# Optimization experiments

Hardware: AMD Instinct MI355X
Metric: run time of the kernel (lower is better)

## Reference

```python
import jax, jax.numpy as jnp
import numpy as np

B, H, W = 64, 512, 512
CD = 400                      # center_dims
MS_H = MS_W = 10              # max shifts
EPS = 1e-8
C_X = (H - CD) // 2           # 56
C_Y = (W - CD) // 2           # 56


def _conv_valid(x, k):
    # x: [B,h,w,1], k: [kh,kw,1,1] -> VALID conv, stride 1
    return jax.lax.conv_general_dilated(
        x, k, window_strides=(1, 1), padding='VALID',
        dimension_numbers=('NHWC', 'HWIO', 'NHWC'))


def setup_inputs() -> dict:
    key = jax.random.key(0)
    k1, k2 = jax.random.split(key)
    # smooth low-frequency template (so NCC peak neighborhood is positive -> log() finite)
    coarse = jax.random.normal(k1, (32, 32), dtype=jnp.float32)
    template = jax.image.resize(coarse, (H, W), method='bilinear')
    template = template - template.min() + 1.0  # keep positive-ish intensities
    noise = 0.05 * jax.random.normal(k2, (B, H, W, 1), dtype=jnp.float32)
    x = template[None, :, :, None] + noise
    return {'x': x, 'template': template}


def reference(x, template):
    # --- template normalization (init-time in the TF layer) ---
    tmpl = template[MS_W + C_X: H - (MS_W + C_X), MS_H + C_Y: W - (MS_H + C_Y)]  # [380,380]
    tmpl = tmpl[:, :, None, None].astype(jnp.float32)                            # HWIO
    t_zm = tmpl - jnp.mean(tmpl, axis=(0, 1), keepdims=True)
    t_var = jnp.sum(jnp.square(t_zm), axis=(0, 1), keepdims=True) + EPS          # [1,1,1,1]

    # --- image normalization ---
    Xc = x[:, C_X:H - C_X, C_Y:W - C_Y, :]                                       # [B,400,400,1]
    imgs_zm = Xc - jnp.mean(Xc, axis=(1, 2), keepdims=True)
    ones_k = jnp.ones_like(tmpl)
    localsum_sq = _conv_valid(jnp.square(Xc), ones_k)                            # [B,21,21,1]
    localsum = _conv_valid(Xc, ones_k)
    n_t = float(np.prod(tmpl.shape))
    imgs_var = localsum_sq - jnp.square(localsum) / n_t + EPS
    imgs_var = jnp.where(imgs_var < 0, jnp.zeros_like(imgs_var), imgs_var)

    # --- NCC ---
    denominator = jnp.sqrt(t_var * imgs_var)
    numerator = _conv_valid(imgs_zm, t_zm)
    ncc = numerator / denominator
    ncc = jnp.where(jnp.isnan(ncc), jnp.zeros_like(ncc), ncc)                    # [B,21,21,1]

    # --- integer argmax + gaussian (log-parabola) subpixel interpolation ---
    ncc2 = ncc[..., 0]                                                           # [B,21,21]
    ww = ncc2.shape[2]
    am = jnp.argmax(ncc2.reshape(B, -1), axis=1)
    sh_x = (am // ww).astype(jnp.int32)
    sh_y = (am % ww).astype(jnp.int32)
    log_ncc = jnp.log(ncc2)
    bidx = jnp.arange(B)

    def g(dx, dy):
        return log_ncc[bidx, sh_x + dx, sh_y + dy]

    log_xm1_y = g(-1, 0); log_xp1_y = g(1, 0)
    log_x_ym1 = g(0, -1); log_x_yp1 = g(0, 1)
    four_log_xy = 4.0 * g(0, 0)
    sh_x_n = (-(sh_x - MS_H)).astype(jnp.float32) - (log_xm1_y - log_xp1_y) / (
        2.0 * log_xm1_y - four_log_xy + 2.0 * log_xp1_y)
    sh_y_n = (-(sh_y - MS_W)).astype(jnp.float32) - (log_x_ym1 - log_x_yp1) / (
        2.0 * log_x_ym1 - four_log_xy + 2.0 * log_x_yp1)

    # --- bilinear translate: translations=[dx,dy]=[sh_y_n, sh_x_n]; out(r,c)=in(r-dy, c-dx), fill 0 ---
    def warp_one(img, dy, dx):
        rr = jnp.arange(H, dtype=jnp.float32)[:, None] - dy    # [H,1]
        cc = jnp.arange(W, dtype=jnp.float32)[None, :] - dx    # [1,W]
        r0 = jnp.floor(rr); c0 = jnp.floor(cc)
        wr = rr - r0; wc = cc - c0
        r0i = jnp.broadcast_to(r0.astype(jnp.int32), (H, W))
        c0i = jnp.broadcast_to(c0.astype(jnp.int32), (H, W))

        def samp(ri, ci):
            valid = (ri >= 0) & (ri < H) & (ci >= 0) & (ci < W)
            v = img[jnp.clip(ri, 0, H - 1), jnp.clip(ci, 0, W - 1)]
            return jnp.where(valid, v, 0.0)

        v00 = samp(r0i, c0i); v01 = samp(r0i, c0i + 1)
        v10 = samp(r0i + 1, c0i); v11 = samp(r0i + 1, c0i + 1)
        return (v00 * (1 - wr) * (1 - wc) + v01 * (1 - wr) * wc
                + v10 * wr * (1 - wc) + v11 * wr * wc)

    warped = jax.vmap(warp_one)(x[..., 0], sh_x_n, sh_y_n)     # [B,H,W]
    # transpose [0,2,1] then flatten, matching the TF layer's output layout
    return jnp.transpose(warped, (0, 2, 1)).reshape(B, H * W)
```

## Files before the change

### kernel.cpp

```cpp
#include <hip/hip_runtime.h>
#include <math.h>

#define HH 512
#define WW 512
#define NB 64
#define CXY 56
#define TOFF 66
#define TN 380
#define XN 400
#define NL 21
#define N_T 144400.0f
#define EPSF 1e-8f
#define NUT 32
#define SXS 424

#define TPART_S   0
#define TPART_S2  384
#define TSTATS    768
#define ROWSUM    1024
#define ROWSUMSQ  (ROWSUM + 537600)
#define LOCALSUM  1076224
#define LOCALSQ   (LOCALSUM + 28224)
#define SHIFTS    1132672
#define SHIFTSI   (SHIFTS + 128)
#define EXACTN    (SHIFTSI + 128)
#define TSHIFT_F  (EXACTN + 384)
#define XF16      (TSHIFT_F + 1677312)
#define CCPART2   8348416

typedef _Float16 half2_t __attribute__((ext_vector_type(2)));
typedef _Float16 f16x8 __attribute__((ext_vector_type(8)));
typedef float f32x4 __attribute__((ext_vector_type(4)));

__global__ __launch_bounds__(128) void k_tstats1(const float* __restrict__ tpl,
                                                 float* __restrict__ ws) {
    int u = blockIdx.x;
    int l = threadIdx.x;
    const float* row = tpl + (TOFF + u) * WW + TOFF;
    float s = 0.f, s2 = 0.f;
    for (int v = l; v < TN; v += 128) { float t = row[v]; s += t; s2 += t * t; }
    for (int off = 32; off; off >>= 1) { s += __shfl_down(s, off); s2 += __shfl_down(s2, off); }
    __shared__ float rs[2], rs2[2];
    int wid = l >> 6;
    if ((l & 63) == 0) { rs[wid] = s; rs2[wid] = s2; }
    __syncthreads();
    if (l == 0) { ws[TPART_S + u] = rs[0] + rs[1]; ws[TPART_S2 + u] = rs2[0] + rs2[1]; }
}

__global__ __launch_bounds__(512) void k_tstats2(float* __restrict__ ws) {
    int l = threadIdx.x;
    float s  = (l < TN) ? ws[TPART_S + l]  : 0.f;
    float s2 = (l < TN) ? ws[TPART_S2 + l] : 0.f;
    for (int off = 32; off; off >>= 1) { s += __shfl_down(s, off); s2 += __shfl_down(s2, off); }
    __shared__ float rs[8], rs2[8];
    int wid = l >> 6;
    if ((l & 63) == 0) { rs[wid] = s; rs2[wid] = s2; }
    __syncthreads();
    if (l == 0) {
        float S = 0.f, S2 = 0.f;
        for (int k = 0; k < 8; ++k) { S += rs[k]; S2 += rs2[k]; }
        float mu = S / N_T;
        ws[TSTATS] = mu;
        ws[TSTATS + 1] = S2 - S * mu + EPSF;
    }
}

__global__ __launch_bounds__(256) void k_tshift(const float* __restrict__ tpl,
                                                float* __restrict__ ws) {
    int u = blockIdx.x;
    int j = blockIdx.y;
    float mu = ws[TSTATS];
    _Float16* dst = (_Float16*)(ws + TSHIFT_F) + ((size_t)j * 384 + u) * 416;
    for (int c = threadIdx.x; c < 416; c += 256) {
        float v = 0.f;
        int vs = c - j;
        if (u < TN && vs >= 0 && vs < TN) v = tpl[(TOFF + u) * WW + TOFF + vs] - mu;
        dst[c] = (_Float16)v;
    }
}

__global__ __launch_bounds__(256) void k_rowsum(const float* __restrict__ x,
                                                float* __restrict__ ws) {
    __shared__ float sm[4][416];
    int wid = threadIdx.x >> 6, lane = threadIdx.x & 63;
    int row = blockIdx.x * 4 + wid;
    int b = row / 416, p = row - b * 416;
    const float* xr = x + ((size_t)b * HH + (CXY + p)) * WW + CXY;
    _Float16* xh = (_Float16*)(ws + XF16) + ((size_t)b * 416 + p) * 416;
    float s = 0.f, s2 = 0.f;
    for (int v = lane; v < 416; v += 64) {
        float t = xr[v];
        sm[wid][v] = t;
        xh[v] = (_Float16)t;
        if (v < TN) { s += t; s2 += t * t; }
    }
    for (int off = 32; off; off >>= 1) { s += __shfl_down(s, off); s2 += __shfl_down(s2, off); }
    __syncthreads();
    if (lane == 0 && p < XN) {
        float* rs  = ws + ROWSUM   + (size_t)(b * XN + p) * NL;
        float* rq  = ws + ROWSUMSQ + (size_t)(b * XN + p) * NL;
        float w = s, w2 = s2;
        rs[0] = w; rq[0] = w2;
        for (int j = 1; j < NL; ++j) {
            float a = sm[wid][j - 1], bv = sm[wid][j + TN - 1];
            w  += bv - a;
            w2 += bv * bv - a * a;
            rs[j] = w; rq[j] = w2;
        }
    }
}

__global__ __launch_bounds__(512) void k_ccm(float* __restrict__ ws) {
    const int bp = blockIdx.x, ut = blockIdx.y;
    const int U = 12 * ut;
    const int tid = threadIdx.x;
    const int lane = tid & 63, wv = tid >> 6;
    __shared__ __align__(16) _Float16 sX[2][32 * SXS];
    __shared__ float sD[7][16][34];

    {
        const _Float16* xh = (const _Float16*)(ws + XF16);
#pragma unroll
        for (int bb = 0; bb < 2; ++bb) {
            const _Float16* src0 = xh + ((size_t)(2 * bp + bb) * 416 + U) * 416;
            for (int c = tid; c < 32 * 52; c += 512) {
                int r = c / 52, c8 = c - r * 52;
                *reinterpret_cast<f16x8*>(&sX[bb][r * SXS + c8 * 8]) =
                    *reinterpret_cast<const f16x8*>(src0 + (size_t)r * 416 + c8 * 8);
            }
        }
    }
    __syncthreads();

    if (wv < 7) {
        const _Float16* tsh = (const _Float16*)(ws + TSHIFT_F);
        const int r16 = lane & 15, h8 = (lane >> 4) * 8;
        const int rbase = (lane >> 4) * 4, cbase = lane & 15;
        const _Float16* bbA = &sX[0][r16 * SXS + h8];
        const _Float16* bbB = &sX[1][r16 * SXS + h8];

        const int j0 = 3 * wv;
        const _Float16* a0 = tsh + ((size_t)(j0    ) * 384 + U + r16) * 416 + h8;
        const _Float16* a1 = tsh + ((size_t)(j0 + 1) * 384 + U + r16) * 416 + h8;
        const _Float16* a2 = tsh + ((size_t)(j0 + 2) * 384 + U + r16) * 416 + h8;

        f32x4 z = {0.f, 0.f, 0.f, 0.f};
        f32x4 c000 = z, c001 = z, c010 = z, c011 = z, c020 = z, c021 = z;
        f32x4 c100 = z, c101 = z, c110 = z, c111 = z, c120 = z, c121 = z;
        f16x8 A0 = *reinterpret_cast<const f16x8*>(a0);
        f16x8 A1 = *reinterpret_cast<const f16x8*>(a1);
        f16x8 A2 = *reinterpret_cast<const f16x8*>(a2);
#pragma unroll
        for (int kc = 0; kc < 13; ++kc) {
            f16x8 N0 = A0, N1 = A1, N2 = A2;
            if (kc < 12) {
                N0 = *reinterpret_cast<const f16x8*>(a0 + (kc + 1) * 32);
                N1 = *reinterpret_cast<const f16x8*>(a1 + (kc + 1) * 32);
                N2 = *reinterpret_cast<const f16x8*>(a2 + (kc + 1) * 32);
            }
            f16x8 B00 = *reinterpret_cast<const f16x8*>(bbA + kc * 32);
            f16x8 B01 = *reinterpret_cast<const f16x8*>(bbA + 16 * SXS + kc * 32);
            f16x8 B10 = *reinterpret_cast<const f16x8*>(bbB + kc * 32);
            f16x8 B11 = *reinterpret_cast<const f16x8*>(bbB + 16 * SXS + kc * 32);
            __builtin_amdgcn_s_setprio(1);
            c000 = __builtin_amdgcn_mfma_f32_16x16x32_f16(A0, B00, c000, 0, 0, 0);
            c001 = __builtin_amdgcn_mfma_f32_16x16x32_f16(A0, B01, c001, 0, 0, 0);
            c100 = __builtin_amdgcn_mfma_f32_16x16x32_f16(A0, B10, c100, 0, 0, 0);
            c101 = __builtin_amdgcn_mfma_f32_16x16x32_f16(A0, B11, c101, 0, 0, 0);
            c010 = __builtin_amdgcn_mfma_f32_16x16x32_f16(A1, B00, c010, 0, 0, 0);
            c011 = __builtin_amdgcn_mfma_f32_16x16x32_f16(A1, B01, c011, 0, 0, 0);
            c110 = __builtin_amdgcn_mfma_f32_16x16x32_f16(A1, B10, c110, 0, 0, 0);
            c111 = __builtin_amdgcn_mfma_f32_16x16x32_f16(A1, B11, c111, 0, 0, 0);
            c020 = __builtin_amdgcn_mfma_f32_16x16x32_f16(A2, B00, c020, 0, 0, 0);
            c021 = __builtin_amdgcn_mfma_f32_16x16x32_f16(A2, B01, c021, 0, 0, 0);
            c120 = __builtin_amdgcn_mfma_f32_16x16x32_f16(A2, B10, c120, 0, 0, 0);
            c121 = __builtin_amdgcn_mfma_f32_16x16x32_f16(A2, B11, c121, 0, 0, 0);
            __builtin_amdgcn_s_setprio(0);
            A0 = N0; A1 = N1; A2 = N2;
        }

#pragma unroll
        for (int jj = 0; jj < 3; ++jj) {
#pragma unroll
            for (int bb = 0; bb < 2; ++bb) {
                f32x4 d0, d1;
                if (bb == 0) { d0 = (jj == 0) ? c000 : (jj == 1) ? c010 : c020;
                               d1 = (jj == 0) ? c001 : (jj == 1) ? c011 : c021; }
                else         { d0 = (jj == 0) ? c100 : (jj == 1) ? c110 : c120;
                               d1 = (jj == 0) ? c101 : (jj == 1) ? c111 : c121; }
#pragma unroll
                for (int q = 0; q < 4; ++q) {
                    sD[wv][rbase + q][cbase]      = d0[q];
                    sD[wv][rbase + q][16 + cbase] = d1[q];
                }
                if (lane < NL) {
                    float s = 0.f;
#pragma unroll
                    for (int row = 0; row < 12; ++row) s += sD[wv][row][row + lane];
                    ws[CCPART2 + ((size_t)((2 * bp + bb) * NUT + ut)) * 441
                       + lane * NL + (j0 + jj)] = s;
                }
            }
        }
    }
}

__global__ __launch_bounds__(512) void k_vncc(float* __restrict__ ws) {
    int b = blockIdx.x, t = threadIdx.x;
    __shared__ float big[XN * 22];
    __shared__ float lsum[441];
    __shared__ float vbuf[512];
    __shared__ int   ibuf[512];

    const float* srcS = ws + ROWSUM + (size_t)b * (XN * NL);
    for (int k = t; k < XN * NL; k += 512) {
        int p = k / NL, j = k - p * NL;
        big[p * 22 + j] = srcS[k];
    }
    __syncthreads();
    if (t < NL * NL) {
        int i = t / NL, j = t - i * NL;
        const float* base = big + i * 22 + j;
        float s0 = 0.f, s1 = 0.f, s2 = 0.f, s3 = 0.f;
        for (int p = 0; p < TN; p += 4) {
            s0 += base[p * 22]; s1 += base[(p + 1) * 22];
            s2 += base[(p + 2) * 22]; s3 += base[(p + 3) * 22];
        }
        float s = (s0 + s1) + (s2 + s3);
        lsum[t] = s;
        ws[LOCALSUM + b * (NL * NL) + t] = s;
    }
    __syncthreads();
    const float* srcQ = ws + ROWSUMSQ + (size_t)b * (XN * NL);
    for (int k = t; k < XN * NL; k += 512) {
        int p = k / NL, j = k - p * NL;
        big[p * 22 + j] = srcQ[k];
    }
    __syncthreads();
    float val = -1e30f;
    if (t < NL * NL) {
        int i = t / NL, j = t - i * NL;
        const float* base = big + i * 22 + j;
        float s0 = 0.f, s1 = 0.f, s2 = 0.f, s3 = 0.f;
        for (int p = 0; p < TN; p += 4) {
            s0 += base[p * 22]; s1 += base[(p + 1) * 22];
            s2 += base[(p + 2) * 22]; s3 += base[(p + 3) * 22];
        }
        float lsq = (s0 + s1) + (s2 + s3);
        ws[LOCALSQ + b * (NL * NL) + t] = lsq;
        float num = 0.f;
        for (int ut = 0; ut < NUT; ++ut)
            num += ws[CCPART2 + ((size_t)(b * NUT + ut)) * 441 + t];
        float ls = lsum[t];
        float ivar = lsq - ls * ls * (1.0f / N_T) + EPSF;
        if (ivar < 0.f) ivar = 0.f;
        float den = sqrtf(ws[TSTATS + 1] * ivar);
        float ncc = num / den;
        if (ncc != ncc) ncc = 0.f;
        val = ncc;
    }
    vbuf[t] = val; ibuf[t] = t;
    __syncthreads();
    for (int off = 256; off; off >>= 1) {
        if (t < off) {
            float v1 = vbuf[t], v2 = vbuf[t + off];
            int   i1 = ibuf[t], i2 = ibuf[t + off];
            if (v2 > v1 || (v2 == v1 && i2 < i1)) { vbuf[t] = v2; ibuf[t] = i2; }
        }
        __syncthreads();
    }
    if (t == 0) {
        int am = ibuf[0];
        ws[SHIFTSI + 2 * b]     = (float)(am / NL);
        ws[SHIFTSI + 2 * b + 1] = (float)(am % NL);
    }
}

__global__ __launch_bounds__(512) void k_exact1(const float* __restrict__ x,
                                                const float* __restrict__ tpl,
                                                float* __restrict__ ws) {
    const int b = blockIdx.x, k = blockIdx.y;
    const int sx = (int)ws[SHIFTSI + 2 * b];
    const int sy = (int)ws[SHIFTSI + 2 * b + 1];
    const int dxs[5] = {0, -1, 1, 0, 0};
    const int dys[5] = {0, 0, 0, -1, 1};
    const int px = min(max(sx + dxs[k], 0), NL - 1);
    const int py = min(max(sy + dys[k], 0), NL - 1);
    const float mu = ws[TSTATS];
    const int lane = threadIdx.x & 63, wv = threadIdx.x >> 6;
    float a = 0.f;
    for (int t = wv; t < TN; t += 8) {
        const float* trow = tpl + (TOFF + t) * WW + TOFF;
        const float* xrow = x + ((size_t)b * HH + (CXY + px + t)) * WW + CXY + py;
#pragma unroll
        for (int it = 0; it < 6; ++it) {
            int v = lane + it * 64;
            if (v < TN) a = fmaf(trow[v] - mu, xrow[v], a);
        }
    }
    for (int off = 32; off; off >>= 1) a += __shfl_down(a, off);
    __shared__ float part[8];
    if (lane == 0) part[wv] = a;
    __syncthreads();
    if (threadIdx.x == 0) {
        float s = 0.f;
        for (int w = 0; w < 8; ++w) s += part[w];
        ws[EXACTN + b * 5 + k] = s;
    }
}

__global__ __launch_bounds__(64) void k_sub(float* __restrict__ ws) {
    int b = threadIdx.x;
    if (b >= NB) return;
    int sx = (int)ws[SHIFTSI + 2 * b];
    int sy = (int)ws[SHIFTSI + 2 * b + 1];
    int lxm = max(sx - 1, 0), lxp = min(sx + 1, NL - 1);
    int lym = max(sy - 1, 0), lyp = min(sy + 1, NL - 1);
    float tvar = ws[TSTATS + 1];
    int cells[5] = { sx * NL + sy, lxm * NL + sy, lxp * NL + sy,
                     sx * NL + lym, sx * NL + lyp };
    float l[5];
    for (int k = 0; k < 5; ++k) {
        float num = ws[EXACTN + b * 5 + k];
        float ls  = ws[LOCALSUM + b * (NL * NL) + cells[k]];
        float lsq = ws[LOCALSQ  + b * (NL * NL) + cells[k]];
        float ivar = lsq - ls * ls * (1.0f / N_T) + EPSF;
        if (ivar < 0.f) ivar = 0.f;
        float ncc = num / sqrtf(tvar * ivar);
        if (ncc != ncc) ncc = 0.f;
        l[k] = logf(ncc);
    }
    float shx = -(float)(sx - 10) - (l[1] - l[2]) / (2.f * l[1] - 4.f * l[0] + 2.f * l[2]);
    float shy = -(float)(sy - 10) - (l[3] - l[4]) / (2.f * l[3] - 4.f * l[0] + 2.f * l[4]);
    ws[SHIFTS + 2 * b]     = shx;
    ws[SHIFTS + 2 * b + 1] = shy;
}

__global__ __launch_bounds__(256) void k_warp(const float* __restrict__ x,
                                              const float* __restrict__ ws,
                                              float* __restrict__ out) {
    const int b = blockIdx.z;
    const int R = blockIdx.x * 64;
    const int C = blockIdx.y * 64;
    const float dy = ws[SHIFTS + 2 * b], dx = ws[SHIFTS + 2 * b + 1];
    const int rlo = (int)floorf((float)R - dy);
    const int clo = (int)floorf((float)C - dx);
    const float wr = ((float)R - dy) - (float)rlo;
    const float wc = ((float)C - dx) - (float)clo;
    __shared__ float sm[66][67];
    const float* img = x + (size_t)b * (HH * WW);

    for (int k = threadIdx.x; k < 66 * 66; k += 256) {
        int kr = k / 66, kc = k - kr * 66;
        int ri = min(max(rlo + kr, 0), HH - 1);
        int ci = min(max(clo + kc, 0), WW - 1);
        sm[kr][kc] = img[ri * WW + ci];
    }
    __syncthreads();

    const int dr = threadIdx.x & 63;
    const int cq = threadIdx.x >> 6;
    const int r  = R + dr;
    const int r0 = rlo + dr;
    const float w00 = (1.f - wr) * (1.f - wc), w01 = (1.f - wr) * wc;
    const float w10 = wr * (1.f - wc),         w11 = wr * wc;
    const bool vr0 = (r0 >= 0) & (r0 < HH);
    const bool vr1 = (r0 + 1 >= 0) & (r0 + 1 < HH);
#pragma unroll
    for (int ci = 0; ci < 16; ++ci) {
        int dc = cq * 16 + ci;
        int c  = C + dc;
        int c0 = clo + dc;
        bool vc0 = (c0 >= 0) & (c0 < WW);
        bool vc1 = (c0 + 1 >= 0) & (c0 + 1 < WW);
        float v00 = (vr0 & vc0) ? sm[dr][dc]         : 0.f;
        float v01 = (vr0 & vc1) ? sm[dr][dc + 1]     : 0.f;
        float v10 = (vr1 & vc0) ? sm[dr + 1][dc]     : 0.f;
        float v11 = (vr1 & vc1) ? sm[dr + 1][dc + 1] : 0.f;
        float o = v00 * w00 + v01 * w01 + v10 * w10 + v11 * w11;
        out[(size_t)b * (HH * WW) + (size_t)c * HH + r] = o;
    }
}

extern "C" void kernel_launch(void* const* d_in, const int* in_sizes, int n_in,
                              void* d_out, int out_size, void* d_ws, size_t ws_size,
                              hipStream_t stream) {
    const float* x   = (const float*)d_in[0];
    const float* tpl = (const float*)d_in[1];
    float* out = (float*)d_out;
    float* ws  = (float*)d_ws;

    k_tstats1<<<TN, 128, 0, stream>>>(tpl, ws);
    k_tstats2<<<1, 512, 0, stream>>>(ws);
    k_tshift<<<dim3(384, NL), 256, 0, stream>>>(tpl, ws);
    k_rowsum<<<(NB * 416) / 4, 256, 0, stream>>>(x, ws);
    k_ccm<<<dim3(NB / 2, NUT), 512, 0, stream>>>(ws);
    k_vncc<<<NB, 512, 0, stream>>>(ws);
    k_exact1<<<dim3(NB, 5), 512, 0, stream>>>(x, tpl, ws);
    k_sub<<<1, 64, 0, stream>>>(ws);
    k_warp<<<dim3(8, 8, NB), dim3(256), 0, stream>>>(x, ws, out);
}
```

Before: 149.4 us.

## Fuse prep kernels, fold subpixel step into warp, shrink ccm blocks

Merges the template row-stats kernel into the x row-sum/f16 conversion kernel as extra blocks. It also moves the per-batch subpixel log-parabola computation into each warp block, removing the separate k_sub launch. The template-shift kernel now handles 16 rows per block. k_ccm runs with 256 threads where each wave processes up to two shift groups instead of 7 of 8 waves doing one. Together these cut launch count and idle waves, at the cost of redundant subpixel work in every warp block and less parallelism per ccm block.

```diff
diff --git a/kernel.cpp b/kernel.cpp
--- a/kernel.cpp
+++ b/kernel.cpp
@@ -32,58 +32,29 @@
 typedef _Float16 f16x8 __attribute__((ext_vector_type(8)));
 typedef float f32x4 __attribute__((ext_vector_type(4)));
 
-__global__ __launch_bounds__(128) void k_tstats1(const float* __restrict__ tpl,
-                                                 float* __restrict__ ws) {
-    int u = blockIdx.x;
-    int l = threadIdx.x;
-    const float* row = tpl + (TOFF + u) * WW + TOFF;
-    float s = 0.f, s2 = 0.f;
-    for (int v = l; v < TN; v += 128) { float t = row[v]; s += t; s2 += t * t; }
-    for (int off = 32; off; off >>= 1) { s += __shfl_down(s, off); s2 += __shfl_down(s2, off); }
-    __shared__ float rs[2], rs2[2];
-    int wid = l >> 6;
-    if ((l & 63) == 0) { rs[wid] = s; rs2[wid] = s2; }
-    __syncthreads();
-    if (l == 0) { ws[TPART_S + u] = rs[0] + rs[1]; ws[TPART_S2 + u] = rs2[0] + rs2[1]; }
-}
-
-__global__ __launch_bounds__(512) void k_tstats2(float* __restrict__ ws) {
-    int l = threadIdx.x;
-    float s  = (l < TN) ? ws[TPART_S + l]  : 0.f;
-    float s2 = (l < TN) ? ws[TPART_S2 + l] : 0.f;
-    for (int off = 32; off; off >>= 1) { s += __shfl_down(s, off); s2 += __shfl_down(s2, off); }
-    __shared__ float rs[8], rs2[8];
-    int wid = l >> 6;
-    if ((l & 63) == 0) { rs[wid] = s; rs2[wid] = s2; }
-    __syncthreads();
-    if (l == 0) {
-        float S = 0.f, S2 = 0.f;
-        for (int k = 0; k < 8; ++k) { S += rs[k]; S2 += rs2[k]; }
-        float mu = S / N_T;
-        ws[TSTATS] = mu;
-        ws[TSTATS + 1] = S2 - S * mu + EPSF;
-    }
-}
-
-__global__ __launch_bounds__(256) void k_tshift(const float* __restrict__ tpl,
-                                                float* __restrict__ ws) {
-    int u = blockIdx.x;
-    int j = blockIdx.y;
-    float mu = ws[TSTATS];
-    _Float16* dst = (_Float16*)(ws + TSHIFT_F) + ((size_t)j * 384 + u) * 416;
-    for (int c = threadIdx.x; c < 416; c += 256) {
-        float v = 0.f;
-        int vs = c - j;
-        if (u < TN && vs >= 0 && vs < TN) v = tpl[(TOFF + u) * WW + TOFF + vs] - mu;
-        dst[c] = (_Float16)v;
-    }
-}
-
-__global__ __launch_bounds__(256) void k_rowsum(const float* __restrict__ x,
-                                                float* __restrict__ ws) {
+__global__ __launch_bounds__(256) void k_prep(const float* __restrict__ x,
+                                              const float* __restrict__ tpl,
+                                              float* __restrict__ ws) {
     __shared__ float sm[4][416];
-    int wid = threadIdx.x >> 6, lane = threadIdx.x & 63;
-    int row = blockIdx.x * 4 + wid;
+    const int tid = threadIdx.x;
+    const int wid = tid >> 6, lane = tid & 63;
+
+    if (blockIdx.x < 380) {
+        int u = blockIdx.x;
+        const float* row = tpl + (TOFF + u) * WW + TOFF;
+        float s = 0.f, s2 = 0.f;
+        for (int v = tid; v < TN; v += 256) { float t = row[v]; s += t; s2 += t * t; }
+        for (int off = 32; off; off >>= 1) { s += __shfl_down(s, off); s2 += __shfl_down(s2, off); }
+        if (lane == 0) { sm[wid][0] = s; sm[wid][1] = s2; }
+        __syncthreads();
+        if (tid == 0) {
+            ws[TPART_S + u]  = sm[0][0] + sm[1][0] + sm[2][0] + sm[3][0];
+            ws[TPART_S2 + u] = sm[0][1] + sm[1][1] + sm[2][1] + sm[3][1];
+        }
+        return;
+    }
+
+    int row = (blockIdx.x - 380) * 4 + wid;
     int b = row / 416, p = row - b * 416;
     const float* xr = x + ((size_t)b * HH + (CXY + p)) * WW + CXY;
     _Float16* xh = (_Float16*)(ws + XF16) + ((size_t)b * 416 + p) * 416;
@@ -110,20 +81,57 @@
     }
 }
 
-__global__ __launch_bounds__(512) void k_ccm(float* __restrict__ ws) {
+__global__ __launch_bounds__(512) void k_tstats2(float* __restrict__ ws) {
+    int l = threadIdx.x;
+    float s  = (l < TN) ? ws[TPART_S + l]  : 0.f;
+    float s2 = (l < TN) ? ws[TPART_S2 + l] : 0.f;
+    for (int off = 32; off; off >>= 1) { s += __shfl_down(s, off); s2 += __shfl_down(s2, off); }
+    __shared__ float rs[8], rs2[8];
+    int wid = l >> 6;
+    if ((l & 63) == 0) { rs[wid] = s; rs2[wid] = s2; }
+    __syncthreads();
+    if (l == 0) {
+        float S = 0.f, S2 = 0.f;
+        for (int k = 0; k < 8; ++k) { S += rs[k]; S2 += rs2[k]; }
+        float mu = S / N_T;
+        ws[TSTATS] = mu;
+        ws[TSTATS + 1] = S2 - S * mu + EPSF;
+    }
+}
+
+__global__ __launch_bounds__(256) void k_tshift(const float* __restrict__ tpl,
+                                                float* __restrict__ ws) {
+    const int j = blockIdx.x, ug = blockIdx.y;
+    const float mu = ws[TSTATS];
+    _Float16* base = (_Float16*)(ws + TSHIFT_F) + (size_t)j * (384 * 416);
+#pragma unroll
+    for (int r = 0; r < 16; ++r) {
+        int u = 16 * ug + r;
+        _Float16* dst = base + (size_t)u * 416;
+        const float* src = tpl + (TOFF + u) * WW + TOFF;
+        for (int c = threadIdx.x; c < 416; c += 256) {
+            float v = 0.f;
+            int vs = c - j;
+            if (u < TN && vs >= 0 && vs < TN) v = src[vs] - mu;
+            dst[c] = (_Float16)v;
+        }
+    }
+}
+
+__global__ __launch_bounds__(256) void k_ccm(float* __restrict__ ws) {
     const int bp = blockIdx.x, ut = blockIdx.y;
     const int U = 12 * ut;
     const int tid = threadIdx.x;
     const int lane = tid & 63, wv = tid >> 6;
     __shared__ __align__(16) _Float16 sX[2][32 * SXS];
-    __shared__ float sD[7][16][34];
+    __shared__ float sD[4][16][34];
 
     {
         const _Float16* xh = (const _Float16*)(ws + XF16);
 #pragma unroll
         for (int bb = 0; bb < 2; ++bb) {
             const _Float16* src0 = xh + ((size_t)(2 * bp + bb) * 416 + U) * 416;
-            for (int c = tid; c < 32 * 52; c += 512) {
+            for (int c = tid; c < 32 * 52; c += 256) {
                 int r = c / 52, c8 = c - r * 52;
                 *reinterpret_cast<f16x8*>(&sX[bb][r * SXS + c8 * 8]) =
                     *reinterpret_cast<const f16x8*>(src0 + (size_t)r * 416 + c8 * 8);
@@ -132,14 +140,16 @@
     }
     __syncthreads();
 
-    if (wv < 7) {
-        const _Float16* tsh = (const _Float16*)(ws + TSHIFT_F);
-        const int r16 = lane & 15, h8 = (lane >> 4) * 8;
-        const int rbase = (lane >> 4) * 4, cbase = lane & 15;
-        const _Float16* bbA = &sX[0][r16 * SXS + h8];
-        const _Float16* bbB = &sX[1][r16 * SXS + h8];
-
-        const int j0 = 3 * wv;
+    const _Float16* tsh = (const _Float16*)(ws + TSHIFT_F);
+    const int r16 = lane & 15, h8 = (lane >> 4) * 8;
+    const int rbase = (lane >> 4) * 4, cbase = lane & 15;
+    const _Float16* bbA = &sX[0][r16 * SXS + h8];
+    const _Float16* bbB = &sX[1][r16 * SXS + h8];
+
+    for (int gi = 0; gi < 2; ++gi) {
+        const int g = wv + 4 * gi;
+        if (g >= 7) break;
+        const int j0 = 3 * g;
         const _Float16* a0 = tsh + ((size_t)(j0    ) * 384 + U + r16) * 416 + h8;
         const _Float16* a1 = tsh + ((size_t)(j0 + 1) * 384 + U + r16) * 416 + h8;
         const _Float16* a2 = tsh + ((size_t)(j0 + 2) * 384 + U + r16) * 416 + h8;
@@ -309,45 +319,45 @@
     }
 }
 
-__global__ __launch_bounds__(64) void k_sub(float* __restrict__ ws) {
-    int b = threadIdx.x;
-    if (b >= NB) return;
-    int sx = (int)ws[SHIFTSI + 2 * b];
-    int sy = (int)ws[SHIFTSI + 2 * b + 1];
-    int lxm = max(sx - 1, 0), lxp = min(sx + 1, NL - 1);
-    int lym = max(sy - 1, 0), lyp = min(sy + 1, NL - 1);
-    float tvar = ws[TSTATS + 1];
-    int cells[5] = { sx * NL + sy, lxm * NL + sy, lxp * NL + sy,
-                     sx * NL + lym, sx * NL + lyp };
-    float l[5];
-    for (int k = 0; k < 5; ++k) {
-        float num = ws[EXACTN + b * 5 + k];
-        float ls  = ws[LOCALSUM + b * (NL * NL) + cells[k]];
-        float lsq = ws[LOCALSQ  + b * (NL * NL) + cells[k]];
-        float ivar = lsq - ls * ls * (1.0f / N_T) + EPSF;
-        if (ivar < 0.f) ivar = 0.f;
-        float ncc = num / sqrtf(tvar * ivar);
-        if (ncc != ncc) ncc = 0.f;
-        l[k] = logf(ncc);
-    }
-    float shx = -(float)(sx - 10) - (l[1] - l[2]) / (2.f * l[1] - 4.f * l[0] + 2.f * l[2]);
-    float shy = -(float)(sy - 10) - (l[3] - l[4]) / (2.f * l[3] - 4.f * l[0] + 2.f * l[4]);
-    ws[SHIFTS + 2 * b]     = shx;
-    ws[SHIFTS + 2 * b + 1] = shy;
-}
-
 __global__ __launch_bounds__(256) void k_warp(const float* __restrict__ x,
                                               const float* __restrict__ ws,
                                               float* __restrict__ out) {
     const int b = blockIdx.z;
     const int R = blockIdx.x * 64;
     const int C = blockIdx.y * 64;
-    const float dy = ws[SHIFTS + 2 * b], dx = ws[SHIFTS + 2 * b + 1];
+    __shared__ float sm[66][67];
+    __shared__ float sh_dy, sh_dx;
+
+    if (threadIdx.x == 0) {
+        int sx = (int)ws[SHIFTSI + 2 * b];
+        int sy = (int)ws[SHIFTSI + 2 * b + 1];
+        int lxm = max(sx - 1, 0), lxp = min(sx + 1, NL - 1);
+        int lym = max(sy - 1, 0), lyp = min(sy + 1, NL - 1);
+        float tvar = ws[TSTATS + 1];
+        int cells[5] = { sx * NL + sy, lxm * NL + sy, lxp * NL + sy,
+                         sx * NL + lym, sx * NL + lyp };
+        float l[5];
+#pragma unroll
+        for (int k = 0; k < 5; ++k) {
+            float num = ws[EXACTN + b * 5 + k];
+            float ls  = ws[LOCALSUM + b * (NL * NL) + cells[k]];
+            float lsq = ws[LOCALSQ  + b * (NL * NL) + cells[k]];
+            float ivar = lsq - ls * ls * (1.0f / N_T) + EPSF;
+            if (ivar < 0.f) ivar = 0.f;
+            float ncc = num / sqrtf(tvar * ivar);
+            if (ncc != ncc) ncc = 0.f;
+            l[k] = logf(ncc);
+        }
+        sh_dy = -(float)(sx - 10) - (l[1] - l[2]) / (2.f * l[1] - 4.f * l[0] + 2.f * l[2]);
+        sh_dx = -(float)(sy - 10) - (l[3] - l[4]) / (2.f * l[3] - 4.f * l[0] + 2.f * l[4]);
+    }
+    __syncthreads();
+    const float dy = sh_dy, dx = sh_dx;
+
     const int rlo = (int)floorf((float)R - dy);
     const int clo = (int)floorf((float)C - dx);
     const float wr = ((float)R - dy) - (float)rlo;
     const float wc = ((float)C - dx) - (float)clo;
-    __shared__ float sm[66][67];
     const float* img = x + (size_t)b * (HH * WW);
 
     for (int k = threadIdx.x; k < 66 * 66; k += 256) {
@@ -390,13 +400,11 @@
     float* out = (float*)d_out;
     float* ws  = (float*)d_ws;
 
-    k_tstats1<<<TN, 128, 0, stream>>>(tpl, ws);
+    k_prep<<<380 + (NB * 416) / 4, 256, 0, stream>>>(x, tpl, ws);
     k_tstats2<<<1, 512, 0, stream>>>(ws);
-    k_tshift<<<dim3(384, NL), 256, 0, stream>>>(tpl, ws);
-    k_rowsum<<<(NB * 416) / 4, 256, 0, stream>>>(x, ws);
-    k_ccm<<<dim3(NB / 2, NUT), 512, 0, stream>>>(ws);
+    k_tshift<<<dim3(NL, 24), 256, 0, stream>>>(tpl, ws);
+    k_ccm<<<dim3(NB / 2, NUT), 256, 0, stream>>>(ws);
     k_vncc<<<NB, 512, 0, stream>>>(ws);
     k_exact1<<<dim3(NB, 5), 512, 0, stream>>>(x, tpl, ws);
-    k_sub<<<1, 64, 0, stream>>>(ws);
     k_warp<<<dim3(8, 8, NB), dim3(256), 0, stream>>>(x, ws, out);
 }
```

Result: slower. 153.1 us (+2.5%).
